# Performance work log

Hardware: AMD Instinct MI355X
Metric: run time of the kernel (lower is better)

Reference implementation:

```python
import jax, jax.numpy as jnp
import numpy as np

DIM = 1024
HEADS = 16
DIM_HEAD = 64
INNER = HEADS * DIM_HEAD  # 1024
MAX_LEN = 4096
BASE = 10000.0
EPS = 1.1920928955078125e-07  # torch.finfo(float32).eps (RMSNorm eps=None default)


def _rope_tables():
    t = np.arange(MAX_LEN, dtype=np.float32)
    inv_freq = 1.0 / (BASE ** (np.arange(0, DIM_HEAD, 2, dtype=np.float32) / DIM_HEAD))
    freqs = np.einsum('i,j->ij', t, inv_freq)          # [max_len, d/2]
    emb = np.concatenate([freqs, freqs], axis=-1)       # [max_len, d]
    return jnp.asarray(np.sin(emb)), jnp.asarray(np.cos(emb))


def setup_inputs() -> dict:
    key = jax.random.key(0)
    ks = jax.random.split(key, 5)
    x = jax.random.normal(ks[0], (2, 2048, DIM), dtype=jnp.float32)
    norm_w = jnp.ones((DIM,), dtype=jnp.float32)
    # store projection weights as [in, out] (transposed torch Linear weight)
    w_qkv = jax.random.normal(ks[1], (DIM, 3 * INNER), dtype=jnp.float32) * (DIM ** -0.5)
    w_o = jax.random.normal(ks[2], (INNER, DIM), dtype=jnp.float32) * (INNER ** -0.5)
    b_o = jax.random.normal(ks[3], (DIM,), dtype=jnp.float32) * 0.01
    sin, cos = _rope_tables()
    return {"x": x, "norm_w": norm_w, "w_qkv": w_qkv, "w_o": w_o, "b_o": b_o,
            "sin": sin, "cos": cos}


def _rotate_half(t):
    t1, t2 = jnp.split(t, 2, axis=-1)
    return jnp.concatenate([-t2, t1], axis=-1)


def _apply_rope(t, sin, cos):
    # t: [b, h, n, d]; sin/cos: [n, d]
    return t * cos + _rotate_half(t) * sin


def reference(x, norm_w, w_qkv, w_o, b_o, sin, cos):
    b, n, _ = x.shape
    # RMSNorm
    xn = x * jax.lax.rsqrt(jnp.mean(x * x, axis=-1, keepdims=True) + EPS) * norm_w
    # QKV projection
    qkv = xn @ w_qkv                                   # [b, n, 3*inner]
    q, k, v = jnp.split(qkv, 3, axis=-1)
    def to_heads(t):
        return t.reshape(b, n, HEADS, DIM_HEAD).transpose(0, 2, 1, 3)  # [b,h,n,d]
    q, k, v = to_heads(q), to_heads(k), to_heads(v)
    s, c = sin[:n], cos[:n]
    q = _apply_rope(q, s, c)
    k = _apply_rope(k, s, c)
    # causal SDPA
    scale = DIM_HEAD ** -0.5
    scores = jnp.einsum('bhqd,bhkd->bhqk', q, k) * scale
    causal = jnp.tril(jnp.ones((n, n), dtype=bool))
    scores = jnp.where(causal, scores, jnp.finfo(scores.dtype).min)
    attn = jax.nn.softmax(scores, axis=-1)
    out = jnp.einsum('bhqk,bhkd->bhqd', attn, v)
    out = out.transpose(0, 2, 1, 3).reshape(b, n, INNER)
    return out @ w_o + b_o
```

## Files before the change

### kernel.cpp

```cpp
#include <hip/hip_runtime.h>
#include <hip/hip_bf16.h>
#include <stdint.h>
#include <stddef.h>

#define NTOK   2048
#define NHEAD  16
#define DHEAD  64
#define DMODEL 1024
#define NROWS  4096
#define NQKV   3072
#define RMS_EPS 1.1920928955078125e-07f
#define QSCALE 0.1803368801111204f

typedef short bf16x8 __attribute__((ext_vector_type(8)));
typedef float f32x4  __attribute__((ext_vector_type(4)));
typedef unsigned short u16x4 __attribute__((ext_vector_type(4)));

__device__ __forceinline__ unsigned short f2b(float f) {
  unsigned u = __builtin_bit_cast(unsigned, f);
  return (unsigned short)((u + 0x7fffu + ((u >> 16) & 1u)) >> 16);
}

__device__ __forceinline__ unsigned pk2bf(float a, float b) {
  __hip_bfloat162 h = __float22bfloat162_rn(make_float2(a, b));
  unsigned u;
  __builtin_memcpy(&u, &h, 4);
  return u;
}

__device__ __forceinline__ void gl16(const void* g, void* l) {
  __builtin_amdgcn_global_load_lds((__attribute__((address_space(1))) void*)g,
                                   (__attribute__((address_space(3))) void*)l,
                                   16, 0, 0);
}

__global__ __launch_bounds__(256) void k_rmsnorm(const float* __restrict__ x,
                                                 const float* __restrict__ w,
                                                 unsigned short* __restrict__ xn) {
  int row = blockIdx.x;
  int t = threadIdx.x;
  float4 v = ((const float4*)(x + (size_t)row * DMODEL))[t];
  float ss = v.x * v.x + v.y * v.y + v.z * v.z + v.w * v.w;
#pragma unroll
  for (int m = 1; m < 64; m <<= 1) ss += __shfl_xor(ss, m, 64);
  __shared__ float red[4];
  if ((t & 63) == 0) red[t >> 6] = ss;
  __syncthreads();
  float tot = (red[0] + red[1]) + (red[2] + red[3]);
  float rs = rsqrtf(tot * (1.0f / DMODEL) + RMS_EPS);
  float4 wv = ((const float4*)w)[t];
  u16x4 o;
  o.x = f2b(v.x * rs * wv.x);
  o.y = f2b(v.y * rs * wv.y);
  o.z = f2b(v.z * rs * wv.z);
  o.w = f2b(v.w * rs * wv.w);
  *(u16x4*)(xn + (size_t)row * DMODEL + t * 4) = o;
}

__global__ __launch_bounds__(256) void k_transpose_bf16(const float* __restrict__ W,
                                                        unsigned short* __restrict__ Wt,
                                                        int K, int Nw) {
  __shared__ float tile[64][65];
  int bk = blockIdx.x * 64;
  int bn = blockIdx.y * 64;
  int t = threadIdx.x;
  int tr = t >> 4;
  int tc = (t & 15) * 4;
#pragma unroll
  for (int rr = 0; rr < 64; rr += 16) {
    float4 v = *(const float4*)&W[(size_t)(bk + tr + rr) * Nw + bn + tc];
    tile[tr + rr][tc + 0] = v.x;
    tile[tr + rr][tc + 1] = v.y;
    tile[tr + rr][tc + 2] = v.z;
    tile[tr + rr][tc + 3] = v.w;
  }
  __syncthreads();
#pragma unroll
  for (int rr = 0; rr < 64; rr += 16) {
    int n = bn + tr + rr;
    u16x4 o;
    o.x = f2b(tile[tc + 0][tr + rr]);
    o.y = f2b(tile[tc + 1][tr + rr]);
    o.z = f2b(tile[tc + 2][tr + rr]);
    o.w = f2b(tile[tc + 3][tr + rr]);
    *(u16x4*)&Wt[(size_t)n * K + bk + tc] = o;
  }
}

__global__ __launch_bounds__(256) void k_qkv_gemm(
    const unsigned short* __restrict__ A, const unsigned short* __restrict__ Bt,
    const float* __restrict__ sin_t, const float* __restrict__ cos_t,
    unsigned short* __restrict__ Qh, unsigned short* __restrict__ Kh,
    unsigned short* __restrict__ Vh) {
  __shared__ unsigned short As[128 * 32];
  __shared__ unsigned short Bs[128 * 32];
  int bm = blockIdx.x, bn = blockIdx.y;
  int t = threadIdx.x;
  int l = t & 63, w = t >> 6;
  int wr = w >> 1, wc = w & 1;
  int lr = l & 15, lg = l >> 4;
  f32x4 acc[4][4] = {};

  int srow = t >> 2;
  int scho = (t & 3) * 8;
  const unsigned short* Ag = A + (size_t)(bm * 128 + srow) * DMODEL + scho;
  const unsigned short* Bg = Bt + (size_t)(bn * 128 + srow) * DMODEL + scho;
  unsigned short* lA0 = &As[t * 8];
  unsigned short* lA1 = &As[(t + 256) * 8];
  unsigned short* lB0 = &Bs[t * 8];
  unsigned short* lB1 = &Bs[(t + 256) * 8];

  for (int k0 = 0; k0 < DMODEL; k0 += 32) {
    gl16(Ag + k0, lA0);
    gl16(Ag + k0 + 64 * DMODEL, lA1);
    gl16(Bg + k0, lB0);
    gl16(Bg + k0 + 64 * DMODEL, lB1);
    __syncthreads();
    bf16x8 af[4], bfr[4];
#pragma unroll
    for (int i = 0; i < 4; i++)
      af[i] = *(const bf16x8*)&As[(wr * 64 + i * 16 + lr) * 32 + lg * 8];
#pragma unroll
    for (int j = 0; j < 4; j++)
      bfr[j] = *(const bf16x8*)&Bs[(wc * 64 + j * 16 + lr) * 32 + lg * 8];
#pragma unroll
    for (int i = 0; i < 4; i++)
#pragma unroll
      for (int j = 0; j < 4; j++)
        acc[i][j] = __builtin_amdgcn_mfma_f32_16x16x32_bf16(af[i], bfr[j], acc[i][j], 0, 0, 0);
    __syncthreads();
  }

  int nc0 = bn * 128 + wc * 64;
  int which = nc0 >> 10;
  int h = (nc0 & 1023) >> 6;
#pragma unroll
  for (int i = 0; i < 4; i++) {
#pragma unroll
    for (int r = 0; r < 4; r++) {
      int m = bm * 128 + wr * 64 + i * 16 + lg * 4 + r;
      int b = m >> 11;
      int n = m & (NTOK - 1);
      size_t obase = ((size_t)(b * NHEAD + h) * NTOK + n) * DHEAD;
      if (which == 2) {
#pragma unroll
        for (int j = 0; j < 4; j++) Vh[obase + j * 16 + lr] = f2b(acc[i][j][r]);
      } else {
        unsigned short* dst = which ? Kh : Qh;
        float qs = which ? 1.0f : QSCALE;
#pragma unroll
        for (int j = 0; j < 2; j++) {
          int d = j * 16 + lr;
          float t1 = acc[i][j][r];
          float t2 = acc[i][j + 2][r];
          float c1 = cos_t[n * DHEAD + d],      s1 = sin_t[n * DHEAD + d];
          float c2 = cos_t[n * DHEAD + d + 32], s2 = sin_t[n * DHEAD + d + 32];
          dst[obase + d]      = f2b((t1 * c1 - t2 * s1) * qs);
          dst[obase + d + 32] = f2b((t2 * c2 + t1 * s2) * qs);
        }
      }
    }
  }
}

__global__ __launch_bounds__(256, 4) void k_attn(
    const unsigned short* __restrict__ Qh, const unsigned short* __restrict__ Kh,
    const unsigned short* __restrict__ Vh, unsigned short* __restrict__ AO) {
  int bh = blockIdx.x;
  int j  = blockIdx.y;
  int m8 = j & 7, k8 = j >> 3;
  int qt = (k8 == 0) ? 31 - m8 : (k8 == 1) ? m8 : (k8 == 2) ? 23 - m8 : 8 + m8;
  int t = threadIdx.x;
  int l = t & 63, w = t >> 6;
  int lr = l & 15, lg = l >> 4;

  __shared__ unsigned short Ks[2][64 * 64];
  __shared__ unsigned short Vt[2][64 * 64];
  __shared__ unsigned short Ps[4][16 * 64];

  const unsigned short* Qb = Qh + (size_t)bh * NTOK * DHEAD;
  const unsigned short* Kb = Kh + (size_t)bh * NTOK * DHEAD;
  const unsigned short* Vb = Vh + (size_t)bh * NTOK * DHEAD;

  int qrow = qt * 64 + w * 16 + lr;
  bf16x8 aq0 = *(const bf16x8*)&Qb[(size_t)qrow * DHEAD + lg * 8];
  bf16x8 aq1 = *(const bf16x8*)&Qb[(size_t)qrow * DHEAD + 32 + lg * 8];

  f32x4 accO[4] = {};
  float mrow = -1e38f;
  float lsum = 0.f;

  int srow = t >> 3;
  int spc  = t & 7;
  int vr0  = (t >> 3) * 2;

  gl16(Kb + (size_t)srow * DHEAD + (spc ^ (srow & 7)) * 8, &Ks[0][t * 8]);
  gl16(Kb + (size_t)(srow + 32) * DHEAD + (spc ^ ((srow + 32) & 7)) * 8, &Ks[0][(t + 256) * 8]);
  {
    bf16x8 v0 = *(const bf16x8*)&Vb[(size_t)vr0 * DHEAD + spc * 8];
    bf16x8 v1 = *(const bf16x8*)&Vb[(size_t)(vr0 + 1) * DHEAD + spc * 8];
#pragma unroll
    for (int jj = 0; jj < 8; jj++) {
      int d = spc * 8 + jj;
      int sw = ((d & 7) ^ ((d >> 3) & 7)) << 4;
      unsigned pk = (unsigned)(unsigned short)v0[jj] | ((unsigned)(unsigned short)v1[jj] << 16);
      *(unsigned*)((char*)Vt[0] + d * 128 + ((vr0 * 2) ^ sw)) = pk;
    }
  }
  __syncthreads();

  for (int kt = 0; kt <= qt; ++kt) {
    int cur = kt & 1, nxt = cur ^ 1;
    int kv0 = kt * 64;
    bool notlast = (kt < qt);

    bf16x8 pv0, pv1;
    if (notlast) {
      int kvn = kv0 + 64;
      gl16(Kb + (size_t)(kvn + srow) * DHEAD + (spc ^ (srow & 7)) * 8, &Ks[nxt][t * 8]);
      gl16(Kb + (size_t)(kvn + srow + 32) * DHEAD + (spc ^ ((srow + 32) & 7)) * 8,
           &Ks[nxt][(t + 256) * 8]);
      pv0 = *(const bf16x8*)&Vb[(size_t)(kvn + vr0) * DHEAD + spc * 8];
      pv1 = *(const bf16x8*)&Vb[(size_t)(kvn + vr0 + 1) * DHEAD + spc * 8];
    }

    f32x4 s[4];
#pragma unroll
    for (int nf = 0; nf < 4; nf++) {
      int krow = nf * 16 + lr;
      const char* kbase = (const char*)Ks[cur] + krow * 128;
      bf16x8 bk0 = *(const bf16x8*)(kbase + ((lg * 16) ^ ((krow & 7) << 4)));
      bf16x8 bk1 = *(const bf16x8*)(kbase + ((lg * 16 + 64) ^ ((krow & 7) << 4)));
      f32x4 z = {};
      z = __builtin_amdgcn_mfma_f32_16x16x32_bf16(bk0, aq0, z, 0, 0, 0);
      s[nf] = __builtin_amdgcn_mfma_f32_16x16x32_bf16(bk1, aq1, z, 0, 0, 0);
    }

    if (kt == qt) {
      int qr = qt * 64 + w * 16 + lr;
#pragma unroll
      for (int nf = 0; nf < 4; nf++)
#pragma unroll
        for (int r = 0; r < 4; r++)
          if (kv0 + nf * 16 + lg * 4 + r > qr) s[nf][r] = -1e30f;
    }

    float t1m = fmaxf(fmaxf(s[0][0], s[0][1]), s[0][2]);
    float t2m = fmaxf(fmaxf(s[0][3], s[1][0]), s[1][1]);
    float t3m = fmaxf(fmaxf(s[1][2], s[1][3]), s[2][0]);
    float t4m = fmaxf(fmaxf(s[2][1], s[2][2]), s[2][3]);
    float t5m = fmaxf(fmaxf(s[3][0], s[3][1]), s[3][2]);
    float pm = fmaxf(fmaxf(fmaxf(t1m, t2m), t3m), fmaxf(fmaxf(t4m, t5m), s[3][3]));
    pm = fmaxf(pm, __shfl_xor(pm, 16, 64));
    pm = fmaxf(pm, __shfl_xor(pm, 32, 64));
    if (__any(pm > mrow + 8.0f)) {
      float mnew = fmaxf(mrow, pm);
      float corr = exp2f(mrow - mnew);
      mrow = mnew;
      lsum *= corr;
      float c0 = __shfl(corr, lg * 4 + 0, 64);
      float c1 = __shfl(corr, lg * 4 + 1, 64);
      float c2 = __shfl(corr, lg * 4 + 2, 64);
      float c3 = __shfl(corr, lg * 4 + 3, 64);
#pragma unroll
      for (int df = 0; df < 4; df++) {
        accO[df][0] *= c0; accO[df][1] *= c1;
        accO[df][2] *= c2; accO[df][3] *= c3;
      }
    }
    {
      float m = mrow;
      float sum = 0.f;
      char* pw = (char*)Ps[w] + lr * 128;
      int sw = (lr & 7) << 4;
#pragma unroll
      for (int nf = 0; nf < 4; nf++) {
        float p0 = exp2f(s[nf][0] - m);
        float p1 = exp2f(s[nf][1] - m);
        float p2 = exp2f(s[nf][2] - m);
        float p3 = exp2f(s[nf][3] - m);
        sum += (p0 + p1) + (p2 + p3);
        unsigned w0 = pk2bf(p0, p1);
        unsigned w1 = pk2bf(p2, p3);
        *(uint64_t*)(pw + ((nf * 32 + lg * 8) ^ sw)) = (uint64_t)w0 | ((uint64_t)w1 << 32);
      }
      sum += __shfl_xor(sum, 16, 64);
      sum += __shfl_xor(sum, 32, 64);
      lsum += sum;
    }

#pragma unroll
    for (int ks = 0; ks < 2; ks++) {
      const char* pb = (const char*)Ps[w] + lr * 128;
      bf16x8 ap = *(const bf16x8*)(pb + ((lg * 16 + ks * 64) ^ ((lr & 7) << 4)));
#pragma unroll
      for (int df = 0; df < 4; df++) {
        int col = df * 16 + lr;
        int sw = ((col & 7) ^ ((col >> 3) & 7)) << 4;
        bf16x8 bv = *(const bf16x8*)((const char*)Vt[cur] + col * 128 + ((lg * 16 + ks * 64) ^ sw));
        accO[df] = __builtin_amdgcn_mfma_f32_16x16x32_bf16(ap, bv, accO[df], 0, 0, 0);
      }
    }

    if (notlast) {
#pragma unroll
      for (int jj = 0; jj < 8; jj++) {
        int d = spc * 8 + jj;
        int sw = ((d & 7) ^ ((d >> 3) & 7)) << 4;
        unsigned pk = (unsigned)(unsigned short)pv0[jj] | ((unsigned)(unsigned short)pv1[jj] << 16);
        *(unsigned*)((char*)Vt[nxt] + d * 128 + ((vr0 * 2) ^ sw)) = pk;
      }
    }
    __syncthreads();
  }

  int b = bh >> 4, h = bh & 15;
  float li = 1.0f / lsum;
  float l0 = __shfl(li, lg * 4 + 0, 64);
  float l1 = __shfl(li, lg * 4 + 1, 64);
  float l2 = __shfl(li, lg * 4 + 2, 64);
  float l3 = __shfl(li, lg * 4 + 3, 64);
  int qbase = qt * 64 + w * 16;
#pragma unroll
  for (int df = 0; df < 4; df++) {
    int d = df * 16 + lr;
    size_t ob = ((size_t)(b * NTOK + qbase + lg * 4)) * DMODEL + h * DHEAD + d;
    AO[ob + 0 * DMODEL] = f2b(accO[df][0] * l0);
    AO[ob + 1 * DMODEL] = f2b(accO[df][1] * l1);
    AO[ob + 2 * DMODEL] = f2b(accO[df][2] * l2);
    AO[ob + 3 * DMODEL] = f2b(accO[df][3] * l3);
  }
}

__global__ __launch_bounds__(256) void k_out_gemm(
    const unsigned short* __restrict__ A, const unsigned short* __restrict__ Bt,
    const float* __restrict__ bias, float* __restrict__ out) {
  __shared__ unsigned short As[128 * 32];
  __shared__ unsigned short Bs[128 * 32];
  int bm = blockIdx.x, bn = blockIdx.y;
  int t = threadIdx.x;
  int l = t & 63, w = t >> 6;
  int wr = w >> 1, wc = w & 1;
  int lr = l & 15, lg = l >> 4;
  f32x4 acc[4][4] = {};

  int srow = t >> 2;
  int scho = (t & 3) * 8;
  const unsigned short* Ag = A + (size_t)(bm * 128 + srow) * DMODEL + scho;
  const unsigned short* Bg = Bt + (size_t)(bn * 128 + srow) * DMODEL + scho;
  unsigned short* lA0 = &As[t * 8];
  unsigned short* lA1 = &As[(t + 256) * 8];
  unsigned short* lB0 = &Bs[t * 8];
  unsigned short* lB1 = &Bs[(t + 256) * 8];

  for (int k0 = 0; k0 < DMODEL; k0 += 32) {
    gl16(Ag + k0, lA0);
    gl16(Ag + k0 + 64 * DMODEL, lA1);
    gl16(Bg + k0, lB0);
    gl16(Bg + k0 + 64 * DMODEL, lB1);
    __syncthreads();
    bf16x8 af[4], bfr[4];
#pragma unroll
    for (int i = 0; i < 4; i++)
      af[i] = *(const bf16x8*)&As[(wr * 64 + i * 16 + lr) * 32 + lg * 8];
#pragma unroll
    for (int j = 0; j < 4; j++)
      bfr[j] = *(const bf16x8*)&Bs[(wc * 64 + j * 16 + lr) * 32 + lg * 8];
#pragma unroll
    for (int i = 0; i < 4; i++)
#pragma unroll
      for (int j = 0; j < 4; j++)
        acc[i][j] = __builtin_amdgcn_mfma_f32_16x16x32_bf16(af[i], bfr[j], acc[i][j], 0, 0, 0);
    __syncthreads();
  }
  int nc0 = bn * 128 + wc * 64;
#pragma unroll
  for (int i = 0; i < 4; i++)
#pragma unroll
    for (int r = 0; r < 4; r++) {
      int m = bm * 128 + wr * 64 + i * 16 + lg * 4 + r;
      float* orow = out + (size_t)m * DMODEL;
#pragma unroll
      for (int j = 0; j < 4; j++) {
        int col = nc0 + j * 16 + lr;
        orow[col] = acc[i][j][r] + bias[col];
      }
    }
}

extern "C" void kernel_launch(void* const* d_in, const int* in_sizes, int n_in,
                              void* d_out, int out_size, void* d_ws, size_t ws_size,
                              hipStream_t stream) {
  const float* x      = (const float*)d_in[0];
  const float* norm_w = (const float*)d_in[1];
  const float* w_qkv  = (const float*)d_in[2];
  const float* w_o    = (const float*)d_in[3];
  const float* b_o    = (const float*)d_in[4];
  const float* sin_t  = (const float*)d_in[5];
  const float* cos_t  = (const float*)d_in[6];
  float* out = (float*)d_out;

  char* ws = (char*)d_ws;
  unsigned short* xn    = (unsigned short*)(ws + (0u << 20));
  unsigned short* wqkvT = (unsigned short*)(ws + (8u << 20));
  unsigned short* woT   = (unsigned short*)(ws + (14u << 20));
  unsigned short* Qh    = (unsigned short*)(ws + (16u << 20));
  unsigned short* Kh    = (unsigned short*)(ws + (24u << 20));
  unsigned short* Vh    = (unsigned short*)(ws + (32u << 20));
  unsigned short* AO    = (unsigned short*)(ws + (40u << 20));

  hipLaunchKernelGGL(k_rmsnorm, dim3(NROWS), dim3(256), 0, stream, x, norm_w, xn);
  hipLaunchKernelGGL(k_transpose_bf16, dim3(16, 48), dim3(256), 0, stream, w_qkv, wqkvT, DMODEL, NQKV);
  hipLaunchKernelGGL(k_transpose_bf16, dim3(16, 16), dim3(256), 0, stream, w_o, woT, DMODEL, DMODEL);
  hipLaunchKernelGGL(k_qkv_gemm, dim3(32, 24), dim3(256), 0, stream, xn, wqkvT, sin_t, cos_t, Qh, Kh, Vh);
  hipLaunchKernelGGL(k_attn, dim3(32, 32), dim3(256), 0, stream, Qh, Kh, Vh, AO);
  hipLaunchKernelGGL(k_out_gemm, dim3(32, 8), dim3(256), 0, stream, AO, woT, b_o, out);
}
```

Before: 135.7 us.

## Double-buffer LDS in both GEMMs and halve out-projection N tile

Both projection GEMMs now use two LDS buffers, so the global-to-LDS loads for the next K step are issued before the MFMA work on the current step, with one barrier per iteration instead of two. This is meant to overlap memory latency with compute. The output GEMM also shrinks its N tile from 128 to 64 columns, doubling the grid to 512 blocks so more CUs are busy. The costs are twice the LDS per block, which can lower occupancy, and more redundant reads of A in the output GEMM.

```diff
diff --git a/kernel.cpp b/kernel.cpp
--- a/kernel.cpp
+++ b/kernel.cpp
@@ -92,8 +92,8 @@
     const float* __restrict__ sin_t, const float* __restrict__ cos_t,
     unsigned short* __restrict__ Qh, unsigned short* __restrict__ Kh,
     unsigned short* __restrict__ Vh) {
-  __shared__ unsigned short As[128 * 32];
-  __shared__ unsigned short Bs[128 * 32];
+  __shared__ unsigned short As[2][128 * 32];
+  __shared__ unsigned short Bs[2][128 * 32];
   int bm = blockIdx.x, bn = blockIdx.y;
   int t = threadIdx.x;
   int l = t & 63, w = t >> 6;
@@ -105,29 +105,34 @@
   int scho = (t & 3) * 8;
   const unsigned short* Ag = A + (size_t)(bm * 128 + srow) * DMODEL + scho;
   const unsigned short* Bg = Bt + (size_t)(bn * 128 + srow) * DMODEL + scho;
-  unsigned short* lA0 = &As[t * 8];
-  unsigned short* lA1 = &As[(t + 256) * 8];
-  unsigned short* lB0 = &Bs[t * 8];
-  unsigned short* lB1 = &Bs[(t + 256) * 8];
-
-  for (int k0 = 0; k0 < DMODEL; k0 += 32) {
-    gl16(Ag + k0, lA0);
-    gl16(Ag + k0 + 64 * DMODEL, lA1);
-    gl16(Bg + k0, lB0);
-    gl16(Bg + k0 + 64 * DMODEL, lB1);
-    __syncthreads();
+
+  gl16(Ag, &As[0][t * 8]);
+  gl16(Ag + 64 * DMODEL, &As[0][(t + 256) * 8]);
+  gl16(Bg, &Bs[0][t * 8]);
+  gl16(Bg + 64 * DMODEL, &Bs[0][(t + 256) * 8]);
+  __syncthreads();
+
+  for (int i = 0; i < 32; i++) {
+    int cur = i & 1, nxt = cur ^ 1;
+    if (i < 31) {
+      int k1 = (i + 1) * 32;
+      gl16(Ag + k1, &As[nxt][t * 8]);
+      gl16(Ag + k1 + 64 * DMODEL, &As[nxt][(t + 256) * 8]);
+      gl16(Bg + k1, &Bs[nxt][t * 8]);
+      gl16(Bg + k1 + 64 * DMODEL, &Bs[nxt][(t + 256) * 8]);
+    }
     bf16x8 af[4], bfr[4];
 #pragma unroll
-    for (int i = 0; i < 4; i++)
-      af[i] = *(const bf16x8*)&As[(wr * 64 + i * 16 + lr) * 32 + lg * 8];
-#pragma unroll
-    for (int j = 0; j < 4; j++)
-      bfr[j] = *(const bf16x8*)&Bs[(wc * 64 + j * 16 + lr) * 32 + lg * 8];
-#pragma unroll
-    for (int i = 0; i < 4; i++)
-#pragma unroll
-      for (int j = 0; j < 4; j++)
-        acc[i][j] = __builtin_amdgcn_mfma_f32_16x16x32_bf16(af[i], bfr[j], acc[i][j], 0, 0, 0);
+    for (int ii = 0; ii < 4; ii++)
+      af[ii] = *(const bf16x8*)&As[cur][(wr * 64 + ii * 16 + lr) * 32 + lg * 8];
+#pragma unroll
+    for (int jj = 0; jj < 4; jj++)
+      bfr[jj] = *(const bf16x8*)&Bs[cur][(wc * 64 + jj * 16 + lr) * 32 + lg * 8];
+#pragma unroll
+    for (int ii = 0; ii < 4; ii++)
+#pragma unroll
+      for (int jj = 0; jj < 4; jj++)
+        acc[ii][jj] = __builtin_amdgcn_mfma_f32_16x16x32_bf16(af[ii], bfr[jj], acc[ii][jj], 0, 0, 0);
     __syncthreads();
   }
 
@@ -335,45 +340,48 @@
 __global__ __launch_bounds__(256) void k_out_gemm(
     const unsigned short* __restrict__ A, const unsigned short* __restrict__ Bt,
     const float* __restrict__ bias, float* __restrict__ out) {
-  __shared__ unsigned short As[128 * 32];
-  __shared__ unsigned short Bs[128 * 32];
+  __shared__ unsigned short As[2][128 * 32];
+  __shared__ unsigned short Bs[2][64 * 32];
   int bm = blockIdx.x, bn = blockIdx.y;
   int t = threadIdx.x;
   int l = t & 63, w = t >> 6;
   int wr = w >> 1, wc = w & 1;
   int lr = l & 15, lg = l >> 4;
-  f32x4 acc[4][4] = {};
+  f32x4 acc[4][2] = {};
 
   int srow = t >> 2;
   int scho = (t & 3) * 8;
   const unsigned short* Ag = A + (size_t)(bm * 128 + srow) * DMODEL + scho;
-  const unsigned short* Bg = Bt + (size_t)(bn * 128 + srow) * DMODEL + scho;
-  unsigned short* lA0 = &As[t * 8];
-  unsigned short* lA1 = &As[(t + 256) * 8];
-  unsigned short* lB0 = &Bs[t * 8];
-  unsigned short* lB1 = &Bs[(t + 256) * 8];
-
-  for (int k0 = 0; k0 < DMODEL; k0 += 32) {
-    gl16(Ag + k0, lA0);
-    gl16(Ag + k0 + 64 * DMODEL, lA1);
-    gl16(Bg + k0, lB0);
-    gl16(Bg + k0 + 64 * DMODEL, lB1);
+  const unsigned short* Bg = Bt + (size_t)(bn * 64 + srow) * DMODEL + scho;
+
+  gl16(Ag, &As[0][t * 8]);
+  gl16(Ag + 64 * DMODEL, &As[0][(t + 256) * 8]);
+  if (srow < 64) gl16(Bg, &Bs[0][t * 8]);
+  __syncthreads();
+
+  for (int i = 0; i < 32; i++) {
+    int cur = i & 1, nxt = cur ^ 1;
+    if (i < 31) {
+      int k1 = (i + 1) * 32;
+      gl16(Ag + k1, &As[nxt][t * 8]);
+      gl16(Ag + k1 + 64 * DMODEL, &As[nxt][(t + 256) * 8]);
+      if (srow < 64) gl16(Bg + k1, &Bs[nxt][t * 8]);
+    }
+    bf16x8 af[4], bfr[2];
+#pragma unroll
+    for (int ii = 0; ii < 4; ii++)
+      af[ii] = *(const bf16x8*)&As[cur][(wr * 64 + ii * 16 + lr) * 32 + lg * 8];
+#pragma unroll
+    for (int jj = 0; jj < 2; jj++)
+      bfr[jj] = *(const bf16x8*)&Bs[cur][(wc * 32 + jj * 16 + lr) * 32 + lg * 8];
+#pragma unroll
+    for (int ii = 0; ii < 4; ii++)
+#pragma unroll
+      for (int jj = 0; jj < 2; jj++)
+        acc[ii][jj] = __builtin_amdgcn_mfma_f32_16x16x32_bf16(af[ii], bfr[jj], acc[ii][jj], 0, 0, 0);
     __syncthreads();
-    bf16x8 af[4], bfr[4];
-#pragma unroll
-    for (int i = 0; i < 4; i++)
-      af[i] = *(const bf16x8*)&As[(wr * 64 + i * 16 + lr) * 32 + lg * 8];
-#pragma unroll
-    for (int j = 0; j < 4; j++)
-      bfr[j] = *(const bf16x8*)&Bs[(wc * 64 + j * 16 + lr) * 32 + lg * 8];
-#pragma unroll
-    for (int i = 0; i < 4; i++)
-#pragma unroll
-      for (int j = 0; j < 4; j++)
-        acc[i][j] = __builtin_amdgcn_mfma_f32_16x16x32_bf16(af[i], bfr[j], acc[i][j], 0, 0, 0);
-    __syncthreads();
-  }
-  int nc0 = bn * 128 + wc * 64;
+  }
+  int nc0 = bn * 64 + wc * 32;
 #pragma unroll
   for (int i = 0; i < 4; i++)
 #pragma unroll
@@ -381,7 +389,7 @@
       int m = bm * 128 + wr * 64 + i * 16 + lg * 4 + r;
       float* orow = out + (size_t)m * DMODEL;
 #pragma unroll
-      for (int j = 0; j < 4; j++) {
+      for (int j = 0; j < 2; j++) {
         int col = nc0 + j * 16 + lr;
         orow[col] = acc[i][j][r] + bias[col];
       }
@@ -414,5 +422,5 @@
   hipLaunchKernelGGL(k_transpose_bf16, dim3(16, 16), dim3(256), 0, stream, w_o, woT, DMODEL, DMODEL);
   hipLaunchKernelGGL(k_qkv_gemm, dim3(32, 24), dim3(256), 0, stream, xn, wqkvT, sin_t, cos_t, Qh, Kh, Vh);
   hipLaunchKernelGGL(k_attn, dim3(32, 32), dim3(256), 0, stream, Qh, Kh, Vh, AO);
-  hipLaunchKernelGGL(k_out_gemm, dim3(32, 8), dim3(256), 0, stream, AO, woT, b_o, out);
-}
+  hipLaunchKernelGGL(k_out_gemm, dim3(32, 16), dim3(256), 0, stream, AO, woT, b_o, out);
+}
```

Measured after the change: 120.5 us. -11.3%, faster.
